# Optimization experiments

Hardware: AMD Instinct MI355X
Metric: run time of the kernel (lower is better)

The kernel has to match this reference:

```python
import jax, jax.numpy as jnp
import numpy as np

N_NODES = 100000


def _gcn_conv(x, src, dst, w, W, b, n):
    # x: [N, Fin]; src/dst: [E'] (self-loops already appended); w: [E']
    h = x @ W                                   # [N, Fout] linear first (Fout <= Fin)
    deg = jax.ops.segment_sum(w, dst, num_segments=n)          # weighted in-degree
    dinv = jnp.where(deg > 0, jax.lax.rsqrt(jnp.maximum(deg, 1e-12)), 0.0)
    norm = dinv[src] * w * dinv[dst]            # [E'] symmetric normalization
    msg = norm[:, None] * h[src]                # [E', Fout] gather + scale
    out = jax.ops.segment_sum(msg, dst, num_segments=n)        # scatter-add
    return out + b


def setup_inputs() -> dict:
    key = jax.random.key(0)
    k1, k2, k3, k4, k5 = jax.random.split(key, 5)
    N, E, Fin, Fh, Fo = N_NODES, 3200000, 256, 128, 64
    x = jax.random.normal(k1, (N, Fin), dtype=jnp.float32)
    edge_index = jax.random.randint(k2, (2, E), 0, N, dtype=jnp.int64)
    edge_weight = jax.random.uniform(k3, (E,), dtype=jnp.float32)
    W1 = jax.random.normal(k4, (Fin, Fh), dtype=jnp.float32) * (1.0 / np.sqrt(Fin))
    b1 = jnp.zeros((Fh,), dtype=jnp.float32)
    W2 = jax.random.normal(k5, (Fh, Fo), dtype=jnp.float32) * (1.0 / np.sqrt(Fh))
    b2 = jnp.zeros((Fo,), dtype=jnp.float32)
    return {"x": x, "edge_index": edge_index, "edge_weight": edge_weight,
            "W1": W1, "b1": b1, "W2": W2, "b2": b2}


def reference(x, edge_index, edge_weight, W1, b1, W2, b2):
    n = x.shape[0]
    loop = jnp.arange(n, dtype=edge_index.dtype)
    src = jnp.concatenate([edge_index[0], loop])
    dst = jnp.concatenate([edge_index[1], loop])
    w = jnp.concatenate([edge_weight, jnp.ones((n,), dtype=edge_weight.dtype)])
    h = _gcn_conv(x, src, dst, w, W1, b1, n)
    h = jax.nn.relu(h)
    out = _gcn_conv(h, src, dst, w, W2, b2, n)
    return out
```

## Files before the change

### kernel.cpp

```cpp
#include <hip/hip_runtime.h>
#include <hip/hip_bf16.h>


#define FIN 256
#define FH  128
#define FO  64

#define EBLK 8192
#define WFX  33554432.0f
#define WFXI (1.0f / 33554432.0f)

typedef short s16x8 __attribute__((ext_vector_type(8)));
typedef float f32x4 __attribute__((ext_vector_type(4)));

__device__ __forceinline__ float h2f(unsigned int u16) {
  union { unsigned short s; _Float16 h; } c; c.s = (unsigned short)u16;
  return (float)c.h;
}
__device__ __forceinline__ unsigned int f2h(float f) {
  union { _Float16 h; unsigned short s; } c; c.h = (_Float16)f;
  return (unsigned int)c.s;
}
__device__ __forceinline__ unsigned int f2bf(float f) {
  union { float f; unsigned int i; } c; c.f = f;
  unsigned int i = c.i;
  return (i + 0x7FFFu + ((i >> 16) & 1u)) >> 16;
}

__global__ __launch_bounds__(256) void prep_w_kernel(
    const float* __restrict__ W1, const float* __restrict__ W2,
    unsigned short* __restrict__ WT1, unsigned short* __restrict__ WT2) {
  int i = blockIdx.x * 256 + threadIdx.x;
  if (i < FIN * FH) {
    int k = i >> 7, j = i & 127;
    WT1[j * FIN + k] = (unsigned short)f2bf(W1[i]);
  } else {
    int i2 = i - FIN * FH;
    if (i2 < FH * FO) {
      int k = i2 >> 6, j = i2 & 63;
      WT2[j * FH + k] = (unsigned short)f2bf(W2[i2]);
    }
  }
}

__global__ __launch_bounds__(256) void a1hist_gemm1_kernel(
    const int* __restrict__ dst, int* __restrict__ gtable, int E,
    int NBA, int NB,
    const float* __restrict__ X, const unsigned short* __restrict__ WT1,
    unsigned short* __restrict__ H1h, int N, int NBG) {
  __shared__ __align__(16) short XS[64 * 40];
  __shared__ __align__(16) short WTS[128 * 40];
  __shared__ unsigned int bh[392];
  int bid = blockIdx.x;
  int tid = threadIdx.x;
  if (bid < NBA) {
    for (int k = tid; k < NB; k += 256) bh[k] = 0u;
    __syncthreads();
    int e0 = bid * EBLK;
    #pragma unroll 4
    for (int it = 0; it < EBLK / 256; ++it) {
      int e = e0 + it * 256 + tid;
      if (e < E) atomicAdd(&bh[dst[e] >> 8], 1u);
    }
    __syncthreads();
    for (int k = tid; k < NB; k += 256)
      gtable[k * NBA + bid] = (int)bh[k];
    return;
  }
  int g = bid - NBA;
  if (g >= NBG) return;
  int row0 = g * 64;
  int wave = tid >> 6, lane = tid & 63;
  int lr = lane & 15, lq = lane >> 4;
  f32x4 acc[8];
  #pragma unroll
  for (int c = 0; c < 8; ++c) acc[c] = (f32x4)(0.f);

  for (int k0 = 0; k0 < FIN; k0 += 32) {
    {
      int row = tid >> 2, koff = (tid & 3) * 8;
      int gr = row0 + row;
      float4 va = make_float4(0.f, 0.f, 0.f, 0.f), vb = va;
      if (gr < N) {
        va = *(const float4*)(X + (size_t)gr * FIN + k0 + koff);
        vb = *(const float4*)(X + (size_t)gr * FIN + k0 + koff + 4);
      }
      s16x8 hv;
      hv[0] = (short)f2bf(va.x); hv[1] = (short)f2bf(va.y);
      hv[2] = (short)f2bf(va.z); hv[3] = (short)f2bf(va.w);
      hv[4] = (short)f2bf(vb.x); hv[5] = (short)f2bf(vb.y);
      hv[6] = (short)f2bf(vb.z); hv[7] = (short)f2bf(vb.w);
      *(s16x8*)(&XS[row * 40 + koff]) = hv;
    }
    {
      int j = tid >> 1, o = (tid & 1) * 16;
      uint4 v0 = *(const uint4*)(WT1 + (size_t)j * FIN + k0 + o);
      uint4 v1 = *(const uint4*)(WT1 + (size_t)j * FIN + k0 + o + 8);
      *(uint4*)(&WTS[j * 40 + o]) = v0;
      *(uint4*)(&WTS[j * 40 + o + 8]) = v1;
    }
    __syncthreads();
    s16x8 af = *(const s16x8*)(&XS[(wave * 16 + lr) * 40 + lq * 8]);
    #pragma unroll
    for (int c = 0; c < 8; ++c) {
      s16x8 bf = *(const s16x8*)(&WTS[(c * 16 + lr) * 40 + lq * 8]);
      acc[c] = __builtin_amdgcn_mfma_f32_16x16x32_bf16(af, bf, acc[c], 0, 0, 0);
    }
    __syncthreads();
  }
  int orow = row0 + wave * 16 + lq * 4;
  #pragma unroll
  for (int c = 0; c < 8; ++c) {
    #pragma unroll
    for (int r = 0; r < 4; ++r) {
      int gr = orow + r;
      if (gr < N)
        H1h[(size_t)gr * FH + c * 16 + lr] = (unsigned short)f2h(acc[c][r]);
    }
  }
}

__global__ __launch_bounds__(256) void scan1i_kernel(
    int* __restrict__ arr, int* __restrict__ bsum, int L) {
  __shared__ int tot[256];
  int t = threadIdx.x;
  int base = blockIdx.x * 1024 + t * 4;
  int v0 = (base + 0 < L) ? arr[base + 0] : 0;
  int v1 = (base + 1 < L) ? arr[base + 1] : 0;
  int v2 = (base + 2 < L) ? arr[base + 2] : 0;
  int v3 = (base + 3 < L) ? arr[base + 3] : 0;
  int s = v0 + v1 + v2 + v3;
  tot[t] = s;
  __syncthreads();
  for (int off = 1; off < 256; off <<= 1) {
    int y = (t >= off) ? tot[t - off] : 0;
    __syncthreads();
    tot[t] += y;
    __syncthreads();
  }
  int p = tot[t] - s;
  if (t == 255) bsum[blockIdx.x] = tot[255];
  if (base + 0 < L) arr[base + 0] = p; p += v0;
  if (base + 1 < L) arr[base + 1] = p; p += v1;
  if (base + 2 < L) arr[base + 2] = p; p += v2;
  if (base + 3 < L) arr[base + 3] = p;
}

__global__ __launch_bounds__(256) void scan2_kernel(
    int* __restrict__ bsum, int nb) {
  __shared__ int buf[256];
  int t = threadIdx.x;
  int v = (t < nb) ? bsum[t] : 0;
  buf[t] = v;
  __syncthreads();
  for (int off = 1; off < 256; off <<= 1) {
    int y = (t >= off) ? buf[t - off] : 0;
    __syncthreads();
    buf[t] += y;
    __syncthreads();
  }
  if (t < nb) bsum[t] = buf[t] - v;
}

__global__ __launch_bounds__(256) void scan3_kernel(
    int* __restrict__ arr, const int* __restrict__ bsum, int L) {
  int i = blockIdx.x * 256 + threadIdx.x;
  if (i < L) arr[i] += bsum[i >> 10];
}

__global__ __launch_bounds__(256) void a3_bucketize_kernel(
    const int* __restrict__ src, const int* __restrict__ dst,
    const float* __restrict__ w, const int* __restrict__ gtable,
    unsigned long long* __restrict__ bdw, int E, int NBA) {
  __shared__ unsigned int bh[392];
  int bid = blockIdx.x;
  int tid = threadIdx.x;
  for (int k = tid; k < 392; k += 256) bh[k] = 0u;
  __syncthreads();
  int e0 = bid * EBLK;
  #pragma unroll 4
  for (int it = 0; it < EBLK / 256; ++it) {
    int e = e0 + it * 256 + tid;
    if (e < E) {
      int d = dst[e];
      int k = d >> 8;
      unsigned int l = (unsigned int)(d & 255);
      unsigned int r = atomicAdd(&bh[k], 1u);
      int pos = gtable[k * NBA + bid] + (int)r;
      unsigned int lo = (unsigned int)src[e] | (l << 20);
      unsigned long long v = ((unsigned long long)__float_as_uint(w[e]) << 32)
                           | (unsigned long long)lo;
      bdw[pos] = v;
    }
  }
}

__global__ __launch_bounds__(256) void b1_degree_kernel(
    const unsigned long long* __restrict__ bdw,
    const int* __restrict__ gtable, int* __restrict__ rowptr,
    float* __restrict__ dinv, int E, int NBA, int NB, int N) {
  __shared__ unsigned int lcnt[256];
  __shared__ unsigned int lwfx[256];
  __shared__ int sc[256];
  int k = blockIdx.x;
  int t = threadIdx.x;
  lcnt[t] = 0u; lwfx[t] = 0u;
  __syncthreads();
  int base = gtable[k * NBA];
  int end  = (k + 1 < NB) ? gtable[(k + 1) * NBA] : E;
  for (int i = base + t; i < end; i += 256) {
    unsigned long long v = bdw[i];
    unsigned int lo = (unsigned int)v;
    unsigned int l = (lo >> 20) & 0xFFu;
    float wv = __uint_as_float((unsigned int)(v >> 32));
    atomicAdd(&lcnt[l], 1u);
    atomicAdd(&lwfx[l], (unsigned int)(wv * WFX));
  }
  __syncthreads();
  int c = (int)lcnt[t];
  sc[t] = c;
  __syncthreads();
  for (int off = 1; off < 256; off <<= 1) {
    int y = (t >= off) ? sc[t - off] : 0;
    __syncthreads();
    sc[t] += y;
    __syncthreads();
  }
  int excl = sc[t] - c;
  int node = (k << 8) + t;
  if (node < N) {
    rowptr[node] = base + excl;
    float deg = (float)lwfx[t] * WFXI;
    dinv[node] = rsqrtf(1.0f + deg);
  }
  if (k == 0 && t == 0) rowptr[N] = E;
}

__global__ __launch_bounds__(256) void b2_scatter_kernel(
    const unsigned long long* __restrict__ bdw,
    const int* __restrict__ gtable, const int* __restrict__ rowptr,
    const float* __restrict__ dinv, int2* __restrict__ edges,
    int E, int NBA, int NB) {
  __shared__ unsigned int rcnt[256];
  int k = blockIdx.x;
  int t = threadIdx.x;
  rcnt[t] = 0u;
  __syncthreads();
  int base = gtable[k * NBA];
  int end  = (k + 1 < NB) ? gtable[(k + 1) * NBA] : E;
  for (int i = base + t; i < end; i += 256) {
    unsigned long long v = bdw[i];
    unsigned int lo = (unsigned int)v;
    int s = (int)(lo & 0xFFFFFu);
    unsigned int l = (lo >> 20) & 0xFFu;
    float wv = __uint_as_float((unsigned int)(v >> 32));
    unsigned int r = atomicAdd(&rcnt[l], 1u);
    int d = (k << 8) + (int)l;
    int pos = rowptr[d] + (int)r;
    float nm = dinv[s] * wv * dinv[d];
    edges[pos] = make_int2(s, __float_as_int(nm));
  }
}

__global__ __launch_bounds__(256) void gemm2_kernel(
    const unsigned short* __restrict__ A1b, const unsigned short* __restrict__ WT2,
    unsigned short* __restrict__ H2h, int N) {
  __shared__ __align__(16) short XS[64 * 40];
  __shared__ __align__(16) short WTS[64 * 40];
  int tid = threadIdx.x;
  int row0 = blockIdx.x * 64;
  int wave = tid >> 6, lane = tid & 63;
  int lr = lane & 15, lq = lane >> 4;
  f32x4 acc[4];
  #pragma unroll
  for (int c = 0; c < 4; ++c) acc[c] = (f32x4)(0.f);

  for (int k0 = 0; k0 < FH; k0 += 32) {
    {
      int row = tid >> 2, o = (tid & 3) * 8;
      int gr = row0 + row;
      uint4 v = make_uint4(0u, 0u, 0u, 0u);
      if (gr < N) v = *(const uint4*)(A1b + (size_t)gr * FH + k0 + o);
      *(uint4*)(&XS[row * 40 + o]) = v;
    }
    {
      int j = tid >> 2, o = (tid & 3) * 8;
      uint4 v = *(const uint4*)(WT2 + (size_t)j * FH + k0 + o);
      *(uint4*)(&WTS[j * 40 + o]) = v;
    }
    __syncthreads();
    s16x8 af = *(const s16x8*)(&XS[(wave * 16 + lr) * 40 + lq * 8]);
    #pragma unroll
    for (int c = 0; c < 4; ++c) {
      s16x8 bf = *(const s16x8*)(&WTS[(c * 16 + lr) * 40 + lq * 8]);
      acc[c] = __builtin_amdgcn_mfma_f32_16x16x32_bf16(af, bf, acc[c], 0, 0, 0);
    }
    __syncthreads();
  }
  int orow = row0 + wave * 16 + lq * 4;
  #pragma unroll
  for (int c = 0; c < 4; ++c) {
    #pragma unroll
    for (int r = 0; r < 4; ++r) {
      int gr = orow + r;
      if (gr < N)
        H2h[(size_t)gr * FO + c * 16 + lr] = (unsigned short)f2h(acc[c][r]);
    }
  }
}

__global__ __launch_bounds__(256) void agg1_kernel(
    const unsigned short* __restrict__ H1h, const int2* __restrict__ edges,
    const int* __restrict__ rowptr, const float* __restrict__ dinv,
    const float* __restrict__ b1, unsigned short* __restrict__ A1b, int N) {
  int wid = (blockIdx.x * 256 + threadIdx.x) >> 6;
  int lane = threadIdx.x & 63;
  if (wid >= N) return;
  int p0 = rowptr[wid], p1 = rowptr[wid + 1];
  int grp = lane >> 4, li = lane & 15;
  const size_t rowoff = (size_t)li * 8;
  float a0[8], a1[8];
  #pragma unroll
  for (int j = 0; j < 8; ++j) { a0[j] = 0.f; a1[j] = 0.f; }

  int p = p0;
  for (; p + 8 <= p1; p += 8) {
    int2 e0 = edges[p + grp];
    int2 e1 = edges[p + 4 + grp];
    uint4 h0 = *(const uint4*)(H1h + (size_t)e0.x * FH + rowoff);
    uint4 h1 = *(const uint4*)(H1h + (size_t)e1.x * FH + rowoff);
    float n0 = __int_as_float(e0.y), n1 = __int_as_float(e1.y);
    a0[0] += n0 * h2f(h0.x & 0xffffu); a0[1] += n0 * h2f(h0.x >> 16);
    a0[2] += n0 * h2f(h0.y & 0xffffu); a0[3] += n0 * h2f(h0.y >> 16);
    a0[4] += n0 * h2f(h0.z & 0xffffu); a0[5] += n0 * h2f(h0.z >> 16);
    a0[6] += n0 * h2f(h0.w & 0xffffu); a0[7] += n0 * h2f(h0.w >> 16);
    a1[0] += n1 * h2f(h1.x & 0xffffu); a1[1] += n1 * h2f(h1.x >> 16);
    a1[2] += n1 * h2f(h1.y & 0xffffu); a1[3] += n1 * h2f(h1.y >> 16);
    a1[4] += n1 * h2f(h1.z & 0xffffu); a1[5] += n1 * h2f(h1.z >> 16);
    a1[6] += n1 * h2f(h1.w & 0xffffu); a1[7] += n1 * h2f(h1.w >> 16);
  }
  for (; p + 4 <= p1; p += 4) {
    int2 e0 = edges[p + grp];
    uint4 h0 = *(const uint4*)(H1h + (size_t)e0.x * FH + rowoff);
    float n0 = __int_as_float(e0.y);
    a0[0] += n0 * h2f(h0.x & 0xffffu); a0[1] += n0 * h2f(h0.x >> 16);
    a0[2] += n0 * h2f(h0.y & 0xffffu); a0[3] += n0 * h2f(h0.y >> 16);
    a0[4] += n0 * h2f(h0.z & 0xffffu); a0[5] += n0 * h2f(h0.z >> 16);
    a0[6] += n0 * h2f(h0.w & 0xffffu); a0[7] += n0 * h2f(h0.w >> 16);
  }
  if (p < p1) {
    int q = p + grp;
    int qi = (q < p1) ? q : p;
    int2 e0 = edges[qi];
    float n0 = (q < p1) ? __int_as_float(e0.y) : 0.f;
    uint4 h0 = *(const uint4*)(H1h + (size_t)e0.x * FH + rowoff);
    a0[0] += n0 * h2f(h0.x & 0xffffu); a0[1] += n0 * h2f(h0.x >> 16);
    a0[2] += n0 * h2f(h0.y & 0xffffu); a0[3] += n0 * h2f(h0.y >> 16);
    a0[4] += n0 * h2f(h0.z & 0xffffu); a0[5] += n0 * h2f(h0.z >> 16);
    a0[6] += n0 * h2f(h0.w & 0xffffu); a0[7] += n0 * h2f(h0.w >> 16);
  }
  float s[8];
  #pragma unroll
  for (int j = 0; j < 8; ++j) {
    s[j] = a0[j] + a1[j];
    s[j] += __shfl_xor(s[j], 16);
    s[j] += __shfl_xor(s[j], 32);
  }
  if (lane < 16) {
    float di = dinv[wid], sn = di * di;
    uint4 hs = *(const uint4*)(H1h + (size_t)wid * FH + rowoff);
    s[0] += sn * h2f(hs.x & 0xffffu); s[1] += sn * h2f(hs.x >> 16);
    s[2] += sn * h2f(hs.y & 0xffffu); s[3] += sn * h2f(hs.y >> 16);
    s[4] += sn * h2f(hs.z & 0xffffu); s[5] += sn * h2f(hs.z >> 16);
    s[6] += sn * h2f(hs.w & 0xffffu); s[7] += sn * h2f(hs.w >> 16);
    float4 bv0 = *(const float4*)(b1 + li * 8);
    float4 bv1 = *(const float4*)(b1 + li * 8 + 4);
    s[0] = fmaxf(s[0] + bv0.x, 0.f); s[1] = fmaxf(s[1] + bv0.y, 0.f);
    s[2] = fmaxf(s[2] + bv0.z, 0.f); s[3] = fmaxf(s[3] + bv0.w, 0.f);
    s[4] = fmaxf(s[4] + bv1.x, 0.f); s[5] = fmaxf(s[5] + bv1.y, 0.f);
    s[6] = fmaxf(s[6] + bv1.z, 0.f); s[7] = fmaxf(s[7] + bv1.w, 0.f);
    uint4 pk;
    pk.x = f2bf(s[0]) | (f2bf(s[1]) << 16);
    pk.y = f2bf(s[2]) | (f2bf(s[3]) << 16);
    pk.z = f2bf(s[4]) | (f2bf(s[5]) << 16);
    pk.w = f2bf(s[6]) | (f2bf(s[7]) << 16);
    *(uint4*)(A1b + (size_t)wid * FH + li * 8) = pk;
  }
}

__global__ __launch_bounds__(256) void agg2_kernel(
    const unsigned short* __restrict__ H2h, const int2* __restrict__ edges,
    const int* __restrict__ rowptr, const float* __restrict__ dinv,
    const float* __restrict__ b2, float* __restrict__ OUT, int N) {
  int wid = (blockIdx.x * 256 + threadIdx.x) >> 6;
  int lane = threadIdx.x & 63;
  if (wid >= N) return;
  int p0 = rowptr[wid], p1 = rowptr[wid + 1];
  int grp = lane >> 3, li = lane & 7;
  const size_t rowoff = (size_t)li * 8;
  float a0[8], a1[8];
  #pragma unroll
  for (int j = 0; j < 8; ++j) { a0[j] = 0.f; a1[j] = 0.f; }

  int p = p0;
  for (; p + 16 <= p1; p += 16) {
    int2 e0 = edges[p + grp];
    int2 e1 = edges[p + 8 + grp];
    uint4 h0 = *(const uint4*)(H2h + (size_t)e0.x * FO + rowoff);
    uint4 h1 = *(const uint4*)(H2h + (size_t)e1.x * FO + rowoff);
    float n0 = __int_as_float(e0.y), n1 = __int_as_float(e1.y);
    a0[0] += n0 * h2f(h0.x & 0xffffu); a0[1] += n0 * h2f(h0.x >> 16);
    a0[2] += n0 * h2f(h0.y & 0xffffu); a0[3] += n0 * h2f(h0.y >> 16);
    a0[4] += n0 * h2f(h0.z & 0xffffu); a0[5] += n0 * h2f(h0.z >> 16);
    a0[6] += n0 * h2f(h0.w & 0xffffu); a0[7] += n0 * h2f(h0.w >> 16);
    a1[0] += n1 * h2f(h1.x & 0xffffu); a1[1] += n1 * h2f(h1.x >> 16);
    a1[2] += n1 * h2f(h1.y & 0xffffu); a1[3] += n1 * h2f(h1.y >> 16);
    a1[4] += n1 * h2f(h1.z & 0xffffu); a1[5] += n1 * h2f(h1.z >> 16);
    a1[6] += n1 * h2f(h1.w & 0xffffu); a1[7] += n1 * h2f(h1.w >> 16);
  }
  for (; p + 8 <= p1; p += 8) {
    int2 e0 = edges[p + grp];
    uint4 h0 = *(const uint4*)(H2h + (size_t)e0.x * FO + rowoff);
    float n0 = __int_as_float(e0.y);
    a0[0] += n0 * h2f(h0.x & 0xffffu); a0[1] += n0 * h2f(h0.x >> 16);
    a0[2] += n0 * h2f(h0.y & 0xffffu); a0[3] += n0 * h2f(h0.y >> 16);
    a0[4] += n0 * h2f(h0.z & 0xffffu); a0[5] += n0 * h2f(h0.z >> 16);
    a0[6] += n0 * h2f(h0.w & 0xffffu); a0[7] += n0 * h2f(h0.w >> 16);
  }
  if (p < p1) {
    int q = p + grp;
    int qi = (q < p1) ? q : p;
    int2 e0 = edges[qi];
    float n0 = (q < p1) ? __int_as_float(e0.y) : 0.f;
    uint4 h0 = *(const uint4*)(H2h + (size_t)e0.x * FO + rowoff);
    a0[0] += n0 * h2f(h0.x & 0xffffu); a0[1] += n0 * h2f(h0.x >> 16);
    a0[2] += n0 * h2f(h0.y & 0xffffu); a0[3] += n0 * h2f(h0.y >> 16);
    a0[4] += n0 * h2f(h0.z & 0xffffu); a0[5] += n0 * h2f(h0.z >> 16);
    a0[6] += n0 * h2f(h0.w & 0xffffu); a0[7] += n0 * h2f(h0.w >> 16);
  }
  float s[8];
  #pragma unroll
  for (int j = 0; j < 8; ++j) {
    s[j] = a0[j] + a1[j];
    s[j] += __shfl_xor(s[j], 8);
    s[j] += __shfl_xor(s[j], 16);
    s[j] += __shfl_xor(s[j], 32);
  }
  if (lane < 8) {
    float di = dinv[wid], sn = di * di;
    uint4 hs = *(const uint4*)(H2h + (size_t)wid * FO + rowoff);
    s[0] += sn * h2f(hs.x & 0xffffu); s[1] += sn * h2f(hs.x >> 16);
    s[2] += sn * h2f(hs.y & 0xffffu); s[3] += sn * h2f(hs.y >> 16);
    s[4] += sn * h2f(hs.z & 0xffffu); s[5] += sn * h2f(hs.z >> 16);
    s[6] += sn * h2f(hs.w & 0xffffu); s[7] += sn * h2f(hs.w >> 16);
    float4 bv0 = *(const float4*)(b2 + li * 8);
    float4 bv1 = *(const float4*)(b2 + li * 8 + 4);
    float4 o0 = make_float4(s[0] + bv0.x, s[1] + bv0.y, s[2] + bv0.z, s[3] + bv0.w);
    float4 o1 = make_float4(s[4] + bv1.x, s[5] + bv1.y, s[6] + bv1.z, s[7] + bv1.w);
    *(float4*)(OUT + (size_t)wid * FO + li * 8) = o0;
    *(float4*)(OUT + (size_t)wid * FO + li * 8 + 4) = o1;
  }
}

extern "C" void kernel_launch(void* const* d_in, const int* in_sizes, int n_in,
                              void* d_out, int out_size, void* d_ws, size_t ws_size,
                              hipStream_t stream) {
  const float* x  = (const float*)d_in[0];
  const int*   ei = (const int*)d_in[1];
  const float* ew = (const float*)d_in[2];
  const float* W1 = (const float*)d_in[3];
  const float* b1 = (const float*)d_in[4];
  const float* W2 = (const float*)d_in[5];
  const float* b2 = (const float*)d_in[6];
  float* out = (float*)d_out;

  const int N = in_sizes[0] / FIN;
  const int E = in_sizes[2];
  const int* src = ei;
  const int* dst = ei + E;
  const int NBG = (N + 63) / 64;
  const int NBA = (E + EBLK - 1) / EBLK;
  const int NB  = (N + 255) / 256;
  const int L   = NB * NBA;
  const int nsb = (L + 1023) / 1024;

  char* ws = (char*)d_ws;
  size_t off = 0;
  unsigned short* h1h = (unsigned short*)(ws + off); off += (size_t)N * FH * 2;
  unsigned short* h2h = (unsigned short*)(ws + off); off += (size_t)N * FO * 2;
  unsigned short* a1b = (unsigned short*)(ws + off); off += (size_t)N * FH * 2;
  int2*  edges  = (int2*) (ws + off); off += (size_t)E * 8;
  unsigned long long* bdw = (unsigned long long*)(ws + off); off += (size_t)E * 8;
  int*   gtable = (int*)  (ws + off); off += (((size_t)L * 4) + 15) & ~(size_t)15;
  int*   rowptr = (int*)  (ws + off); off += (((size_t)(N + 1) * 4) + 15) & ~(size_t)15;
  float* dinv   = (float*)(ws + off); off += (size_t)N * 4;
  int*   bsum   = (int*)  (ws + off); off += 1024;
  unsigned short* WT1 = (unsigned short*)(ws + off); off += (size_t)FH * FIN * 2;
  unsigned short* WT2 = (unsigned short*)(ws + off); off += (size_t)FO * FH * 2;

  prep_w_kernel<<<(FIN * FH + FH * FO + 255) / 256, 256, 0, stream>>>(W1, W2, WT1, WT2);
  a1hist_gemm1_kernel<<<NBA + NBG, 256, 0, stream>>>(dst, gtable, E, NBA, NB,
                                                     x, WT1, h1h, N, NBG);
  scan1i_kernel<<<nsb, 256, 0, stream>>>(gtable, bsum, L);
  scan2_kernel<<<1, 256, 0, stream>>>(bsum, nsb);
  scan3_kernel<<<(L + 255) / 256, 256, 0, stream>>>(gtable, bsum, L);
  a3_bucketize_kernel<<<NBA, 256, 0, stream>>>(src, dst, ew, gtable, bdw, E, NBA);
  b1_degree_kernel<<<NB, 256, 0, stream>>>(bdw, gtable, rowptr, dinv, E, NBA, NB, N);
  b2_scatter_kernel<<<NB, 256, 0, stream>>>(bdw, gtable, rowptr, dinv, edges,
                                            E, NBA, NB);
  agg1_kernel<<<(N * 64 + 255) / 256, 256, 0, stream>>>(h1h, edges, rowptr,
                                                        dinv, b1, a1b, N);
  gemm2_kernel<<<(N + 63) / 64, 256, 0, stream>>>(a1b, WT2, h2h, N);
  agg2_kernel<<<(N * 64 + 255) / 256, 256, 0, stream>>>(h2h, edges, rowptr,
                                                        dinv, b2, out, N);
}
```

Baseline: 371.4 us.

## Fuse layer-1 aggregation with second GEMM via shared-memory staging

Merges agg1 and gemm2 into one kernel. Each block aggregates 64 destination nodes, one wave per 16 nodes processed sequentially, and writes the bf16 ReLU activations into LDS, which then feeds the MFMA GEMM directly. This removes the global write and read of the N x 128 intermediate and one kernel launch. In exchange, each wave walks its 16 nodes serially, so there are far fewer concurrent gathers in flight and per-wave latency hiding is lower. The fp16 unpacking is also switched to __half22float2 helpers.

```diff
diff --git a/kernel.cpp b/kernel.cpp
--- a/kernel.cpp
+++ b/kernel.cpp
@@ -1,5 +1,6 @@
 #include <hip/hip_runtime.h>
 #include <hip/hip_bf16.h>
+#include <hip/hip_fp16.h>
 
 
 #define FIN 256
@@ -25,6 +26,14 @@
   union { float f; unsigned int i; } c; c.f = f;
   unsigned int i = c.i;
   return (i + 0x7FFFu + ((i >> 16) & 1u)) >> 16;
+}
+__device__ __forceinline__ void cvt8(const uint4& v, float* f) {
+  const __half2* hp = (const __half2*)&v;
+  #pragma unroll
+  for (int j = 0; j < 4; ++j) {
+    float2 t = __half22float2(hp[j]);
+    f[2 * j] = t.x; f[2 * j + 1] = t.y;
+  }
 }
 
 __global__ __launch_bounds__(256) void prep_w_kernel(
@@ -262,129 +271,120 @@
   }
 }
 
-__global__ __launch_bounds__(256) void gemm2_kernel(
-    const unsigned short* __restrict__ A1b, const unsigned short* __restrict__ WT2,
+__global__ __launch_bounds__(256) void agg1_gemm2_kernel(
+    const unsigned short* __restrict__ H1h, const int2* __restrict__ edges,
+    const int* __restrict__ rowptr, const float* __restrict__ dinv,
+    const float* __restrict__ b1, const unsigned short* __restrict__ WT2,
     unsigned short* __restrict__ H2h, int N) {
-  __shared__ __align__(16) short XS[64 * 40];
+  __shared__ __align__(16) short AS[64 * 136];
   __shared__ __align__(16) short WTS[64 * 40];
   int tid = threadIdx.x;
+  int wave = tid >> 6, lane = tid & 63;
   int row0 = blockIdx.x * 64;
-  int wave = tid >> 6, lane = tid & 63;
-  int lr = lane & 15, lq = lane >> 4;
+  int grp = lane >> 4, li = lane & 15;
+  const size_t rowoff = (size_t)li * 8;
+
+  for (int i = 0; i < 16; ++i) {
+    int node = row0 + wave * 16 + i;
+    int p0 = 0, p1 = 0;
+    if (node < N) { p0 = rowptr[node]; p1 = rowptr[node + 1]; }
+    float a0[8], a1v[8];
+    #pragma unroll
+    for (int j = 0; j < 8; ++j) { a0[j] = 0.f; a1v[j] = 0.f; }
+    int p = p0;
+    for (; p + 8 <= p1; p += 8) {
+      int2 e0 = edges[p + grp];
+      int2 e1 = edges[p + 4 + grp];
+      uint4 h0 = *(const uint4*)(H1h + (size_t)e0.x * FH + rowoff);
+      uint4 h1 = *(const uint4*)(H1h + (size_t)e1.x * FH + rowoff);
+      float n0 = __int_as_float(e0.y), n1 = __int_as_float(e1.y);
+      float f0[8], f1[8];
+      cvt8(h0, f0); cvt8(h1, f1);
+      #pragma unroll
+      for (int j = 0; j < 8; ++j) {
+        a0[j] += n0 * f0[j];
+        a1v[j] += n1 * f1[j];
+      }
+    }
+    for (; p + 4 <= p1; p += 4) {
+      int2 e0 = edges[p + grp];
+      uint4 h0 = *(const uint4*)(H1h + (size_t)e0.x * FH + rowoff);
+      float n0 = __int_as_float(e0.y);
+      float f0[8];
+      cvt8(h0, f0);
+      #pragma unroll
+      for (int j = 0; j < 8; ++j) a0[j] += n0 * f0[j];
+    }
+    if (p < p1) {
+      int q = p + grp;
+      int qi = (q < p1) ? q : p;
+      int2 e0 = edges[qi];
+      float n0 = (q < p1) ? __int_as_float(e0.y) : 0.f;
+      uint4 h0 = *(const uint4*)(H1h + (size_t)e0.x * FH + rowoff);
+      float f0[8];
+      cvt8(h0, f0);
+      #pragma unroll
+      for (int j = 0; j < 8; ++j) a0[j] += n0 * f0[j];
+    }
+    float s[8];
+    #pragma unroll
+    for (int j = 0; j < 8; ++j) {
+      s[j] = a0[j] + a1v[j];
+      s[j] += __shfl_xor(s[j], 16);
+      s[j] += __shfl_xor(s[j], 32);
+    }
+    if (lane < 16) {
+      uint4 pk = make_uint4(0u, 0u, 0u, 0u);
+      if (node < N) {
+        float di = dinv[node], sn = di * di;
+        uint4 hs = *(const uint4*)(H1h + (size_t)node * FH + rowoff);
+        float fs[8];
+        cvt8(hs, fs);
+        #pragma unroll
+        for (int j = 0; j < 8; ++j) s[j] += sn * fs[j];
+        float4 bv0 = *(const float4*)(b1 + li * 8);
+        float4 bv1 = *(const float4*)(b1 + li * 8 + 4);
+        s[0] = fmaxf(s[0] + bv0.x, 0.f); s[1] = fmaxf(s[1] + bv0.y, 0.f);
+        s[2] = fmaxf(s[2] + bv0.z, 0.f); s[3] = fmaxf(s[3] + bv0.w, 0.f);
+        s[4] = fmaxf(s[4] + bv1.x, 0.f); s[5] = fmaxf(s[5] + bv1.y, 0.f);
+        s[6] = fmaxf(s[6] + bv1.z, 0.f); s[7] = fmaxf(s[7] + bv1.w, 0.f);
+        pk.x = f2bf(s[0]) | (f2bf(s[1]) << 16);
+        pk.y = f2bf(s[2]) | (f2bf(s[3]) << 16);
+        pk.z = f2bf(s[4]) | (f2bf(s[5]) << 16);
+        pk.w = f2bf(s[6]) | (f2bf(s[7]) << 16);
+      }
+      *(uint4*)(&AS[(wave * 16 + i) * 136 + li * 8]) = pk;
+    }
+  }
+  __syncthreads();
+
   f32x4 acc[4];
   #pragma unroll
   for (int c = 0; c < 4; ++c) acc[c] = (f32x4)(0.f);
-
   for (int k0 = 0; k0 < FH; k0 += 32) {
-    {
-      int row = tid >> 2, o = (tid & 3) * 8;
-      int gr = row0 + row;
-      uint4 v = make_uint4(0u, 0u, 0u, 0u);
-      if (gr < N) v = *(const uint4*)(A1b + (size_t)gr * FH + k0 + o);
-      *(uint4*)(&XS[row * 40 + o]) = v;
-    }
     {
       int j = tid >> 2, o = (tid & 3) * 8;
       uint4 v = *(const uint4*)(WT2 + (size_t)j * FH + k0 + o);
       *(uint4*)(&WTS[j * 40 + o]) = v;
     }
     __syncthreads();
-    s16x8 af = *(const s16x8*)(&XS[(wave * 16 + lr) * 40 + lq * 8]);
+    s16x8 af = *(const s16x8*)(&AS[(wave * 16 + li) * 136 + k0 + grp * 8]);
     #pragma unroll
     for (int c = 0; c < 4; ++c) {
-      s16x8 bf = *(const s16x8*)(&WTS[(c * 16 + lr) * 40 + lq * 8]);
+      s16x8 bf = *(const s16x8*)(&WTS[(c * 16 + li) * 40 + grp * 8]);
       acc[c] = __builtin_amdgcn_mfma_f32_16x16x32_bf16(af, bf, acc[c], 0, 0, 0);
     }
     __syncthreads();
   }
-  int orow = row0 + wave * 16 + lq * 4;
+  int orow = row0 + wave * 16 + grp * 4;
   #pragma unroll
   for (int c = 0; c < 4; ++c) {
     #pragma unroll
     for (int r = 0; r < 4; ++r) {
       int gr = orow + r;
       if (gr < N)
-        H2h[(size_t)gr * FO + c * 16 + lr] = (unsigned short)f2h(acc[c][r]);
-    }
-  }
-}
-
-__global__ __launch_bounds__(256) void agg1_kernel(
-    const unsigned short* __restrict__ H1h, const int2* __restrict__ edges,
-    const int* __restrict__ rowptr, const float* __restrict__ dinv,
-    const float* __restrict__ b1, unsigned short* __restrict__ A1b, int N) {
-  int wid = (blockIdx.x * 256 + threadIdx.x) >> 6;
-  int lane = threadIdx.x & 63;
-  if (wid >= N) return;
-  int p0 = rowptr[wid], p1 = rowptr[wid + 1];
-  int grp = lane >> 4, li = lane & 15;
-  const size_t rowoff = (size_t)li * 8;
-  float a0[8], a1[8];
-  #pragma unroll
-  for (int j = 0; j < 8; ++j) { a0[j] = 0.f; a1[j] = 0.f; }
-
-  int p = p0;
-  for (; p + 8 <= p1; p += 8) {
-    int2 e0 = edges[p + grp];
-    int2 e1 = edges[p + 4 + grp];
-    uint4 h0 = *(const uint4*)(H1h + (size_t)e0.x * FH + rowoff);
-    uint4 h1 = *(const uint4*)(H1h + (size_t)e1.x * FH + rowoff);
-    float n0 = __int_as_float(e0.y), n1 = __int_as_float(e1.y);
-    a0[0] += n0 * h2f(h0.x & 0xffffu); a0[1] += n0 * h2f(h0.x >> 16);
-    a0[2] += n0 * h2f(h0.y & 0xffffu); a0[3] += n0 * h2f(h0.y >> 16);
-    a0[4] += n0 * h2f(h0.z & 0xffffu); a0[5] += n0 * h2f(h0.z >> 16);
-    a0[6] += n0 * h2f(h0.w & 0xffffu); a0[7] += n0 * h2f(h0.w >> 16);
-    a1[0] += n1 * h2f(h1.x & 0xffffu); a1[1] += n1 * h2f(h1.x >> 16);
-    a1[2] += n1 * h2f(h1.y & 0xffffu); a1[3] += n1 * h2f(h1.y >> 16);
-    a1[4] += n1 * h2f(h1.z & 0xffffu); a1[5] += n1 * h2f(h1.z >> 16);
-    a1[6] += n1 * h2f(h1.w & 0xffffu); a1[7] += n1 * h2f(h1.w >> 16);
-  }
-  for (; p + 4 <= p1; p += 4) {
-    int2 e0 = edges[p + grp];
-    uint4 h0 = *(const uint4*)(H1h + (size_t)e0.x * FH + rowoff);
-    float n0 = __int_as_float(e0.y);
-    a0[0] += n0 * h2f(h0.x & 0xffffu); a0[1] += n0 * h2f(h0.x >> 16);
-    a0[2] += n0 * h2f(h0.y & 0xffffu); a0[3] += n0 * h2f(h0.y >> 16);
-    a0[4] += n0 * h2f(h0.z & 0xffffu); a0[5] += n0 * h2f(h0.z >> 16);
-    a0[6] += n0 * h2f(h0.w & 0xffffu); a0[7] += n0 * h2f(h0.w >> 16);
-  }
-  if (p < p1) {
-    int q = p + grp;
-    int qi = (q < p1) ? q : p;
-    int2 e0 = edges[qi];
-    float n0 = (q < p1) ? __int_as_float(e0.y) : 0.f;
-    uint4 h0 = *(const uint4*)(H1h + (size_t)e0.x * FH + rowoff);
-    a0[0] += n0 * h2f(h0.x & 0xffffu); a0[1] += n0 * h2f(h0.x >> 16);
-    a0[2] += n0 * h2f(h0.y & 0xffffu); a0[3] += n0 * h2f(h0.y >> 16);
-    a0[4] += n0 * h2f(h0.z & 0xffffu); a0[5] += n0 * h2f(h0.z >> 16);
-    a0[6] += n0 * h2f(h0.w & 0xffffu); a0[7] += n0 * h2f(h0.w >> 16);
-  }
-  float s[8];
-  #pragma unroll
-  for (int j = 0; j < 8; ++j) {
-    s[j] = a0[j] + a1[j];
-    s[j] += __shfl_xor(s[j], 16);
-    s[j] += __shfl_xor(s[j], 32);
-  }
-  if (lane < 16) {
-    float di = dinv[wid], sn = di * di;
-    uint4 hs = *(const uint4*)(H1h + (size_t)wid * FH + rowoff);
-    s[0] += sn * h2f(hs.x & 0xffffu); s[1] += sn * h2f(hs.x >> 16);
-    s[2] += sn * h2f(hs.y & 0xffffu); s[3] += sn * h2f(hs.y >> 16);
-    s[4] += sn * h2f(hs.z & 0xffffu); s[5] += sn * h2f(hs.z >> 16);
-    s[6] += sn * h2f(hs.w & 0xffffu); s[7] += sn * h2f(hs.w >> 16);
-    float4 bv0 = *(const float4*)(b1 + li * 8);
-    float4 bv1 = *(const float4*)(b1 + li * 8 + 4);
-    s[0] = fmaxf(s[0] + bv0.x, 0.f); s[1] = fmaxf(s[1] + bv0.y, 0.f);
-    s[2] = fmaxf(s[2] + bv0.z, 0.f); s[3] = fmaxf(s[3] + bv0.w, 0.f);
-    s[4] = fmaxf(s[4] + bv1.x, 0.f); s[5] = fmaxf(s[5] + bv1.y, 0.f);
-    s[6] = fmaxf(s[6] + bv1.z, 0.f); s[7] = fmaxf(s[7] + bv1.w, 0.f);
-    uint4 pk;
-    pk.x = f2bf(s[0]) | (f2bf(s[1]) << 16);
-    pk.y = f2bf(s[2]) | (f2bf(s[3]) << 16);
-    pk.z = f2bf(s[4]) | (f2bf(s[5]) << 16);
-    pk.w = f2bf(s[6]) | (f2bf(s[7]) << 16);
-    *(uint4*)(A1b + (size_t)wid * FH + li * 8) = pk;
+        H2h[(size_t)gr * FO + c * 16 + li] = (unsigned short)f2h(acc[c][r]);
+    }
   }
 }
 
@@ -398,9 +398,9 @@
   int p0 = rowptr[wid], p1 = rowptr[wid + 1];
   int grp = lane >> 3, li = lane & 7;
   const size_t rowoff = (size_t)li * 8;
-  float a0[8], a1[8];
-  #pragma unroll
-  for (int j = 0; j < 8; ++j) { a0[j] = 0.f; a1[j] = 0.f; }
+  float a0[8], a1v[8];
+  #pragma unroll
+  for (int j = 0; j < 8; ++j) { a0[j] = 0.f; a1v[j] = 0.f; }
 
   int p = p0;
   for (; p + 16 <= p1; p += 16) {
@@ -409,23 +409,22 @@
     uint4 h0 = *(const uint4*)(H2h + (size_t)e0.x * FO + rowoff);
     uint4 h1 = *(const uint4*)(H2h + (size_t)e1.x * FO + rowoff);
     float n0 = __int_as_float(e0.y), n1 = __int_as_float(e1.y);
-    a0[0] += n0 * h2f(h0.x & 0xffffu); a0[1] += n0 * h2f(h0.x >> 16);
-    a0[2] += n0 * h2f(h0.y & 0xffffu); a0[3] += n0 * h2f(h0.y >> 16);
-    a0[4] += n0 * h2f(h0.z & 0xffffu); a0[5] += n0 * h2f(h0.z >> 16);
-    a0[6] += n0 * h2f(h0.w & 0xffffu); a0[7] += n0 * h2f(h0.w >> 16);
-    a1[0] += n1 * h2f(h1.x & 0xffffu); a1[1] += n1 * h2f(h1.x >> 16);
-    a1[2] += n1 * h2f(h1.y & 0xffffu); a1[3] += n1 * h2f(h1.y >> 16);
-    a1[4] += n1 * h2f(h1.z & 0xffffu); a1[5] += n1 * h2f(h1.z >> 16);
-    a1[6] += n1 * h2f(h1.w & 0xffffu); a1[7] += n1 * h2f(h1.w >> 16);
+    float f0[8], f1[8];
+    cvt8(h0, f0); cvt8(h1, f1);
+    #pragma unroll
+    for (int j = 0; j < 8; ++j) {
+      a0[j] += n0 * f0[j];
+      a1v[j] += n1 * f1[j];
+    }
   }
   for (; p + 8 <= p1; p += 8) {
     int2 e0 = edges[p + grp];
     uint4 h0 = *(const uint4*)(H2h + (size_t)e0.x * FO + rowoff);
     float n0 = __int_as_float(e0.y);
-    a0[0] += n0 * h2f(h0.x & 0xffffu); a0[1] += n0 * h2f(h0.x >> 16);
-    a0[2] += n0 * h2f(h0.y & 0xffffu); a0[3] += n0 * h2f(h0.y >> 16);
-    a0[4] += n0 * h2f(h0.z & 0xffffu); a0[5] += n0 * h2f(h0.z >> 16);
-    a0[6] += n0 * h2f(h0.w & 0xffffu); a0[7] += n0 * h2f(h0.w >> 16);
+    float f0[8];
+    cvt8(h0, f0);
+    #pragma unroll
+    for (int j = 0; j < 8; ++j) a0[j] += n0 * f0[j];
   }
   if (p < p1) {
     int q = p + grp;
@@ -433,15 +432,15 @@
     int2 e0 = edges[qi];
     float n0 = (q < p1) ? __int_as_float(e0.y) : 0.f;
     uint4 h0 = *(const uint4*)(H2h + (size_t)e0.x * FO + rowoff);
-    a0[0] += n0 * h2f(h0.x & 0xffffu); a0[1] += n0 * h2f(h0.x >> 16);
-    a0[2] += n0 * h2f(h0.y & 0xffffu); a0[3] += n0 * h2f(h0.y >> 16);
-    a0[4] += n0 * h2f(h0.z & 0xffffu); a0[5] += n0 * h2f(h0.z >> 16);
-    a0[6] += n0 * h2f(h0.w & 0xffffu); a0[7] += n0 * h2f(h0.w >> 16);
+    float f0[8];
+    cvt8(h0, f0);
+    #pragma unroll
+    for (int j = 0; j < 8; ++j) a0[j] += n0 * f0[j];
   }
   float s[8];
   #pragma unroll
   for (int j = 0; j < 8; ++j) {
-    s[j] = a0[j] + a1[j];
+    s[j] = a0[j] + a1v[j];
     s[j] += __shfl_xor(s[j], 8);
     s[j] += __shfl_xor(s[j], 16);
     s[j] += __shfl_xor(s[j], 32);
@@ -449,10 +448,10 @@
   if (lane < 8) {
     float di = dinv[wid], sn = di * di;
     uint4 hs = *(const uint4*)(H2h + (size_t)wid * FO + rowoff);
-    s[0] += sn * h2f(hs.x & 0xffffu); s[1] += sn * h2f(hs.x >> 16);
-    s[2] += sn * h2f(hs.y & 0xffffu); s[3] += sn * h2f(hs.y >> 16);
-    s[4] += sn * h2f(hs.z & 0xffffu); s[5] += sn * h2f(hs.z >> 16);
-    s[6] += sn * h2f(hs.w & 0xffffu); s[7] += sn * h2f(hs.w >> 16);
+    float fs[8];
+    cvt8(hs, fs);
+    #pragma unroll
+    for (int j = 0; j < 8; ++j) s[j] += sn * fs[j];
     float4 bv0 = *(const float4*)(b2 + li * 8);
     float4 bv1 = *(const float4*)(b2 + li * 8 + 4);
     float4 o0 = make_float4(s[0] + bv0.x, s[1] + bv0.y, s[2] + bv0.z, s[3] + bv0.w);
@@ -488,7 +487,6 @@
   size_t off = 0;
   unsigned short* h1h = (unsigned short*)(ws + off); off += (size_t)N * FH * 2;
   unsigned short* h2h = (unsigned short*)(ws + off); off += (size_t)N * FO * 2;
-  unsigned short* a1b = (unsigned short*)(ws + off); off += (size_t)N * FH * 2;
   int2*  edges  = (int2*) (ws + off); off += (size_t)E * 8;
   unsigned long long* bdw = (unsigned long long*)(ws + off); off += (size_t)E * 8;
   int*   gtable = (int*)  (ws + off); off += (((size_t)L * 4) + 15) & ~(size_t)15;
@@ -508,9 +506,8 @@
   b1_degree_kernel<<<NB, 256, 0, stream>>>(bdw, gtable, rowptr, dinv, E, NBA, NB, N);
   b2_scatter_kernel<<<NB, 256, 0, stream>>>(bdw, gtable, rowptr, dinv, edges,
                                             E, NBA, NB);
-  agg1_kernel<<<(N * 64 + 255) / 256, 256, 0, stream>>>(h1h, edges, rowptr,
-                                                        dinv, b1, a1b, N);
-  gemm2_kernel<<<(N + 63) / 64, 256, 0, stream>>>(a1b, WT2, h2h, N);
+  agg1_gemm2_kernel<<<NBG, 256, 0, stream>>>(h1h, edges, rowptr, dinv, b1,
+                                             WT2, h2h, N);
   agg2_kernel<<<(N * 64 + 255) / 256, 256, 0, stream>>>(h2h, edges, rowptr,
                                                         dinv, b2, out, N);
 }
```

After: 400.7 us. 7.9% more time.
